# Performance work log

Hardware: AMD Instinct MI355X
Metric: run time of the kernel (lower is better)

Reference implementation:

```python
import jax, jax.numpy as jnp
import numpy as np

N = 100000
E = 6400000
H = 32  # num_hidden


def setup_inputs() -> dict:
    key = jax.random.key(0)
    ks = jax.random.split(key, 10)
    x = jax.random.normal(ks[0], (N,), dtype=jnp.float32)
    u = jax.random.normal(ks[1], (N,), dtype=jnp.float32)
    edge_index = jax.random.randint(ks[2], (2, E), 0, N, dtype=jnp.int64)
    # MLP(2 -> H -> H -> 1), 3 linear layers with relu between
    def lin(k, fan_in, fan_out):
        bound = 1.0 / np.sqrt(fan_in)
        kw, kb = jax.random.split(k)
        W = jax.random.uniform(kw, (fan_in, fan_out), jnp.float32, -bound, bound)
        b = jax.random.uniform(kb, (fan_out,), jnp.float32, -bound, bound)
        return W, b
    W1, b1 = lin(ks[3], 2, H)
    W2, b2 = lin(ks[4], H, H)
    W3, b3 = lin(ks[5], H, 1)
    return {"x": x, "edge_index": edge_index, "u": u,
            "W1": W1, "b1": b1, "W2": W2, "b2": b2, "W3": W3, "b3": b3}


def reference(x, edge_index, u, W1, b1, W2, b2, W3, b3):
    src, dst = edge_index[0], edge_index[1]
    # gather node scalars, form per-edge feature [E, 2]
    x_edge = jnp.stack([x[src], x[dst]], axis=-1)
    # per-edge MLP: 2 -> H -> H -> 1 with relu
    h = jax.nn.relu(x_edge @ W1 + b1)
    h = jax.nn.relu(h @ W2 + b2)
    w = (h @ W3 + b3)[:, 0]  # [E]
    # spmm: f[i] = sum_{e: src[e]=i} w[e] * u[dst[e]]
    f = jax.ops.segment_sum(w * u[dst], src, num_segments=x.shape[0])
    return f
```

## Files before the change

kernel.cpp:

```cpp
#include <hip/hip_runtime.h>

#define H 32
#define NSEG 1000
#define RBITS 9
#define RANGE 512
#define SPLIT 10
#define SEGPER (NSEG / SPLIT)
#define MAXROWS 260
#define EBMAX 6400

typedef __attribute__((ext_vector_type(2))) __fp16 half2v;
typedef __attribute__((ext_vector_type(8))) __fp16 half8;
typedef __attribute__((ext_vector_type(4))) float f32x4;
typedef unsigned int u32;
typedef unsigned short u16;

union HU { int i[4]; half8 h; };

static __device__ __forceinline__ int pkrtz(float a, float b) {
    return __builtin_bit_cast(int, __builtin_amdgcn_cvt_pkrtz(a, b));
}

static __device__ __forceinline__ float fdot2f(int w, int ab, float c) {
    return __builtin_amdgcn_fdot2(__builtin_bit_cast(half2v, w),
                                  __builtin_bit_cast(half2v, ab), c, false);
}

struct Invar {
    int   w1p[8];
    float b1v[8];
    half8 afrag[2];
    f32x4 c0, c1;
    float w3lo[4], w3hi[4];
    float b3v;
};

static __device__ __forceinline__ void load_invar(
    Invar& v, int g, int col,
    const float* __restrict__ W1, const float* __restrict__ b1,
    const float* __restrict__ W2, const float* __restrict__ b2,
    const float* __restrict__ W3, const float* __restrict__ b3)
{
    const int klo = 4 * g, khi = 16 + 4 * g;
#pragma unroll
    for (int i = 0; i < 4; ++i) {
        v.w1p[i]     = pkrtz(W1[klo + i], W1[H + klo + i]);
        v.w1p[4 + i] = pkrtz(W1[khi + i], W1[H + khi + i]);
        v.b1v[i]     = b1[klo + i];
        v.b1v[4 + i] = b1[khi + i];
    }
#pragma unroll
    for (int mt = 0; mt < 2; ++mt) {
        HU ua;
        const int c = mt * 16 + col;
        ua.i[0] = pkrtz(W2[(klo + 0) * H + c], W2[(klo + 1) * H + c]);
        ua.i[1] = pkrtz(W2[(klo + 2) * H + c], W2[(klo + 3) * H + c]);
        ua.i[2] = pkrtz(W2[(khi + 0) * H + c], W2[(khi + 1) * H + c]);
        ua.i[3] = pkrtz(W2[(khi + 2) * H + c], W2[(khi + 3) * H + c]);
        v.afrag[mt] = ua.h;
    }
#pragma unroll
    for (int r = 0; r < 4; ++r) {
        v.c0[r] = b2[klo + r]; v.c1[r] = b2[khi + r];
        v.w3lo[r] = W3[klo + r]; v.w3hi[r] = W3[khi + r];
    }
    v.b3v = b3[0];
}

static __device__ __forceinline__ float edge_w(const Invar& v, int g, int col, int abpk)
{
    float wred0 = 0.f, wred1 = 0.f, wred2 = 0.f, wred3 = 0.f;
#pragma unroll
    for (int T = 0; T < 4; ++T) {
        const int abT = __builtin_amdgcn_ds_bpermute(((T << 4) + col) << 2, abpk);
        const float h0 = fmaxf(fdot2f(v.w1p[0], abT, v.b1v[0]), 0.f);
        const float h1 = fmaxf(fdot2f(v.w1p[1], abT, v.b1v[1]), 0.f);
        const float h2 = fmaxf(fdot2f(v.w1p[2], abT, v.b1v[2]), 0.f);
        const float h3 = fmaxf(fdot2f(v.w1p[3], abT, v.b1v[3]), 0.f);
        const float h4 = fmaxf(fdot2f(v.w1p[4], abT, v.b1v[4]), 0.f);
        const float h5 = fmaxf(fdot2f(v.w1p[5], abT, v.b1v[5]), 0.f);
        const float h6 = fmaxf(fdot2f(v.w1p[6], abT, v.b1v[6]), 0.f);
        const float h7 = fmaxf(fdot2f(v.w1p[7], abT, v.b1v[7]), 0.f);

        HU ub;
        ub.i[0] = pkrtz(h0, h1);
        ub.i[1] = pkrtz(h2, h3);
        ub.i[2] = pkrtz(h4, h5);
        ub.i[3] = pkrtz(h6, h7);

        f32x4 acc0 = __builtin_amdgcn_mfma_f32_16x16x32_f16(v.afrag[0], ub.h, v.c0, 0, 0, 0);
        f32x4 acc1 = __builtin_amdgcn_mfma_f32_16x16x32_f16(v.afrag[1], ub.h, v.c1, 0, 0, 0);

        float p = 0.f;
#pragma unroll
        for (int r = 0; r < 4; ++r) {
            p += fmaxf(acc0[r], 0.f) * v.w3lo[r];
            p += fmaxf(acc1[r], 0.f) * v.w3hi[r];
        }
        p += __shfl_xor(p, 16, 64);
        p += __shfl_xor(p, 32, 64);
        const float wt = p + v.b3v;
        if      (T == 0) wred0 = wt;
        else if (T == 1) wred1 = wt;
        else if (T == 2) wred2 = wt;
        else             wred3 = wt;
    }
    const float wa = (g & 1) ? wred1 : wred0;
    const float wb = (g & 1) ? wred3 : wred2;
    return (g & 2) ? wb : wa;
}

__global__ void xu_pack_kernel(const float* __restrict__ x, const float* __restrict__ u,
                               float2* __restrict__ xu, int n) {
    int i = blockIdx.x * 256 + threadIdx.x;
    if (i < n) xu[i] = make_float2(x[i], u[i]);
}

__global__ __launch_bounds__(256) void p1_kernel(
    const float* __restrict__ x,
    const int*   __restrict__ ei,
    const float2* __restrict__ xu,
    const float* __restrict__ W1, const float* __restrict__ b1,
    const float* __restrict__ W2, const float* __restrict__ b2,
    const float* __restrict__ W3, const float* __restrict__ b3,
    u32* __restrict__ pairs, u32* __restrict__ offs,
    int E, int Eb, int nbuk)
{
    __shared__ u32 cnt[MAXROWS];
    __shared__ u32 cur[MAXROWS];
    __shared__ u32 wsum[4];
    __shared__ u32 lds_pairs[EBMAX];
    const int tid  = threadIdx.x;
    const int lane = tid & 63;
    const int wv   = tid >> 6;
    const int g    = lane >> 4;
    const int col  = lane & 15;
    const int b    = blockIdx.x;

    const int slice0 = b * Eb;
    int sliceN = E - slice0;
    if (sliceN < 0) sliceN = 0;
    if (sliceN > Eb) sliceN = Eb;

    Invar v;
    load_invar(v, g, col, W1, b1, W2, b2, W3, b3);

    for (int k = tid; k <= nbuk; k += 256) cnt[k] = 0;
    __syncthreads();
    if (((slice0 & 3) == 0) && ((sliceN & 3) == 0)) {
        const uint4* e4 = (const uint4*)(ei + slice0);
        const int n4 = sliceN >> 2;
        for (int i = tid; i < n4; i += 256) {
            const uint4 s4 = e4[i];
            atomicAdd(&cnt[s4.x >> RBITS], 1u);
            atomicAdd(&cnt[s4.y >> RBITS], 1u);
            atomicAdd(&cnt[s4.z >> RBITS], 1u);
            atomicAdd(&cnt[s4.w >> RBITS], 1u);
        }
    } else {
        for (int i = tid; i < sliceN; i += 256)
            atomicAdd(&cnt[((u32)ei[slice0 + i]) >> RBITS], 1u);
    }
    __syncthreads();

    {
        const u32 myc = (tid < nbuk) ? cnt[tid] : 0;
        u32 val = myc;
#pragma unroll
        for (int d = 1; d < 64; d <<= 1) {
            const u32 t = __shfl_up(val, d, 64);
            if (lane >= d) val += t;
        }
        if (lane == 63) wsum[wv] = val;
        __syncthreads();
        u32 woff = 0;
#pragma unroll
        for (int w = 0; w < 4; ++w) if (w < wv) woff += wsum[w];
        val += woff;
        if (tid < nbuk) cur[tid] = val - myc;
        if (tid == 0)   cur[nbuk] = wsum[0] + wsum[1] + wsum[2] + wsum[3];
    }
    __syncthreads();
    for (int k = tid; k <= nbuk; k += 256) offs[(size_t)k * NSEG + b] = cur[k];
    __syncthreads();

    const int nbfull = sliceN >> 6;
    const int nquad  = nbfull >> 2;
    for (int q = wv; q < nquad; q += 4) {
        const int e0 = slice0 + (q << 8) + lane;
        const int e1 = e0 + 64, e2 = e0 + 128, e3 = e0 + 192;
        const int src0 = ei[e0],     src1 = ei[e1],     src2 = ei[e2],     src3 = ei[e3];
        const int dst0 = ei[E + e0], dst1 = ei[E + e1], dst2 = ei[E + e2], dst3 = ei[E + e3];
        const float  x0  = x[src0],  x1  = x[src1],  x2  = x[src2],  x3  = x[src3];
        const float2 xd0 = xu[dst0], xd1 = xu[dst1], xd2 = xu[dst2], xd3 = xu[dst3];

        const float w0 = edge_w(v, g, col, pkrtz(x0, xd0.x));
        const float w1 = edge_w(v, g, col, pkrtz(x1, xd1.x));
        const float w2 = edge_w(v, g, col, pkrtz(x2, xd2.x));
        const float w3 = edge_w(v, g, col, pkrtz(x3, xd3.x));

        const u32 pos0 = atomicAdd(&cur[((u32)src0) >> RBITS], 1u);
        lds_pairs[pos0] = ((u32)(u16)pkrtz(w0 * xd0.y, 0.0f)) | (((u32)src0 & (RANGE - 1)) << 16);
        const u32 pos1 = atomicAdd(&cur[((u32)src1) >> RBITS], 1u);
        lds_pairs[pos1] = ((u32)(u16)pkrtz(w1 * xd1.y, 0.0f)) | (((u32)src1 & (RANGE - 1)) << 16);
        const u32 pos2 = atomicAdd(&cur[((u32)src2) >> RBITS], 1u);
        lds_pairs[pos2] = ((u32)(u16)pkrtz(w2 * xd2.y, 0.0f)) | (((u32)src2 & (RANGE - 1)) << 16);
        const u32 pos3 = atomicAdd(&cur[((u32)src3) >> RBITS], 1u);
        lds_pairs[pos3] = ((u32)(u16)pkrtz(w3 * xd3.y, 0.0f)) | (((u32)src3 & (RANGE - 1)) << 16);
    }
    const int nbany = (sliceN + 63) >> 6;
    for (int bi = (nquad << 2) + wv; bi < nbany; bi += 4) {
        const int loc = (bi << 6) + lane;
        const bool valid = loc < sliceN;
        const int eL = slice0 + (valid ? loc : 0);
        const int src = ei[eL];
        const int dst = ei[E + eL];
        const float2 xud = xu[dst];
        const int abpk = pkrtz(x[src], xud.x);
        const float we = edge_w(v, g, col, abpk);
        if (valid) {
            const int buk = ((u32)src) >> RBITS;
            const u32 pos = atomicAdd(&cur[buk], 1u);
            lds_pairs[pos] = ((u32)(u16)pkrtz(we * xud.y, 0.0f)) | (((u32)src & (RANGE - 1)) << 16);
        }
    }
    __syncthreads();

    const int n4 = sliceN >> 2;
    const uint4* lp4 = (const uint4*)lds_pairs;
    uint4* gp4 = (uint4*)(pairs + slice0);
    for (int i = tid; i < n4; i += 256) gp4[i] = lp4[i];
    for (int i = (n4 << 2) + tid; i < sliceN; i += 256) pairs[slice0 + i] = lds_pairs[i];
}

__global__ __launch_bounds__(256) void p2_kernel(
    const u32* __restrict__ pairs, const u32* __restrict__ offs,
    float* __restrict__ pf, int Eb, int nbuk)
{
    __shared__ float acc[RANGE];
    __shared__ u32 so_l[SEGPER];
    __shared__ u32 pre[SEGPER + 1];
    __shared__ u32 wsum[4];
    const int tid = threadIdx.x;
    const int lane = tid & 63;
    const int wv  = tid >> 6;
    const int buk = blockIdx.x / SPLIT;
    const int sp  = blockIdx.x % SPLIT;

    acc[tid] = 0.f;
    acc[tid + 256] = 0.f;
    u32 myc = 0, so = 0;
    if (tid < SEGPER) {
        const int s = sp + tid * SPLIT;
        so  = offs[(size_t)buk * NSEG + s];
        myc = offs[(size_t)(buk + 1) * NSEG + s] - so;
    }
    {
        u32 val = myc;
#pragma unroll
        for (int d = 1; d < 64; d <<= 1) {
            const u32 t = __shfl_up(val, d, 64);
            if (lane >= d) val += t;
        }
        if (lane == 63) wsum[wv] = val;
        __syncthreads();
        u32 woff = 0;
#pragma unroll
        for (int w = 0; w < 4; ++w) if (w < wv) woff += wsum[w];
        val += woff;
        if (tid < SEGPER) { so_l[tid] = so; pre[tid + 1] = val; }
        if (tid == 0) pre[0] = 0;
    }
    __syncthreads();

    const int total = (int)pre[SEGPER];
    for (int base = tid << 2; base < total; base += 1024) {
#pragma unroll
        for (int k = 0; k < 4; ++k) {
            const int i = base + k;
            if (i >= total) break;
            int lo = 0, hi = SEGPER;
            while (hi - lo > 1) {
                const int mid = (lo + hi) >> 1;
                if (pre[mid] <= (u32)i) lo = mid; else hi = mid;
            }
            const int s = sp + lo * SPLIT;
            const u32 p = pairs[(size_t)s * Eb + so_l[lo] + (u32)i - pre[lo]];
            const float val = (float)__builtin_bit_cast(_Float16, (u16)(p & 0xffffu));
            atomicAdd(&acc[p >> 16], val);
        }
    }
    __syncthreads();

    const size_t stride = (size_t)nbuk * RANGE;
    const int node0 = buk * RANGE;
    pf[(size_t)sp * stride + node0 + tid] = acc[tid];
    pf[(size_t)sp * stride + node0 + tid + 256] = acc[tid + 256];
}

__global__ void freduce_kernel(const float* __restrict__ pf, float* __restrict__ f,
                               int n, int stride) {
    const int i = blockIdx.x * 256 + threadIdx.x;
    if (i >= n) return;
    float s = 0.f;
#pragma unroll
    for (int r = 0; r < SPLIT; ++r) s += pf[(size_t)r * stride + i];
    f[i] = s;
}

__global__ void zero_kernel(float* __restrict__ p, int n) {
    int i = blockIdx.x * blockDim.x + threadIdx.x;
    if (i < n) p[i] = 0.0f;
}

__global__ __launch_bounds__(256) void fb_kernel(
    const float* __restrict__ x,
    const int*   __restrict__ ei,
    const float* __restrict__ u,
    const float* __restrict__ W1, const float* __restrict__ b1,
    const float* __restrict__ W2, const float* __restrict__ b2,
    const float* __restrict__ W3, const float* __restrict__ b3,
    float* __restrict__ f, int E)
{
    const int lane = threadIdx.x & 63;
    const int g    = lane >> 4;
    const int col  = lane & 15;

    Invar v;
    load_invar(v, g, col, W1, b1, W2, b2, W3, b3);

    const int nbatch = E >> 6;
    const int gw = blockIdx.x * 4 + (threadIdx.x >> 6);
    const int nw = gridDim.x * 4;
    for (int bt = gw; bt < nbatch; bt += nw) {
        const int e   = (bt << 6) + lane;
        const int src = ei[e];
        const int dst = ei[E + e];
        const int abpk = pkrtz(x[src], x[dst]);
        const float ud = u[dst];
        const float we = edge_w(v, g, col, abpk);
        atomicAdd(&f[src], we * ud);
    }
}

extern "C" void kernel_launch(void* const* d_in, const int* in_sizes, int n_in,
                              void* d_out, int out_size, void* d_ws, size_t ws_size,
                              hipStream_t stream) {
    const float* x  = (const float*)d_in[0];
    const int*   ei = (const int*)d_in[1];
    const float* u  = (const float*)d_in[2];
    const float* W1 = (const float*)d_in[3];
    const float* b1 = (const float*)d_in[4];
    const float* W2 = (const float*)d_in[5];
    const float* b2 = (const float*)d_in[6];
    const float* W3 = (const float*)d_in[7];
    const float* b3 = (const float*)d_in[8];
    float* f = (float*)d_out;

    const int n = in_sizes[0];
    const int E = in_sizes[1] / 2;

    const int nbuk = (n + RANGE - 1) / RANGE;
    const int Eb = (((E + NSEG - 1) / NSEG) + 63) & ~63;
    const size_t stride = (size_t)nbuk * RANGE;
    const size_t need = ((size_t)NSEG * Eb + (size_t)(nbuk + 1) * NSEG + (size_t)SPLIT * stride)
                        * sizeof(u32);
    const bool xu_fits = (size_t)SPLIT * stride * sizeof(float) >= (size_t)n * sizeof(float2);

    if (nbuk + 1 <= MAXROWS && nbuk <= 256 && Eb <= EBMAX && ws_size >= need
        && (E & 63) == 0 && xu_fits) {
        u32* pairs = (u32*)d_ws;
        u32* offs  = pairs + (size_t)NSEG * Eb;
        float* pf  = (float*)(offs + (size_t)(nbuk + 1) * NSEG);
        float2* xu = (float2*)pf;

        xu_pack_kernel<<<(n + 255) / 256, 256, 0, stream>>>(x, u, xu, n);
        p1_kernel<<<NSEG, 256, 0, stream>>>(x, ei, xu, W1, b1, W2, b2, W3, b3,
                                            pairs, offs, E, Eb, nbuk);
        p2_kernel<<<nbuk * SPLIT, 256, 0, stream>>>(pairs, offs, pf, Eb, nbuk);
        freduce_kernel<<<(n + 255) / 256, 256, 0, stream>>>(pf, f, n, (int)stride);
    } else {
        zero_kernel<<<(n + 255) / 256, 256, 0, stream>>>(f, n);
        fb_kernel<<<2048, 256, 0, stream>>>(x, ei, u, W1, b1, W2, b2, W3, b3, f, E);
    }
}
```

Before: 127.4 us.

## Split fused MLP+bucket-sort kernel into separate MLP and sort kernels

The fused p1 kernel, which computed per-edge MLP weights and bucket-sorted them in LDS, is split in two. A new mlp_kernel runs without the large LDS footprint on 2048 blocks and writes packed fp16 values to global memory. A separate sort_kernel then reads src and those values back and scatters them into bucket order. This aims to raise occupancy for the compute-heavy MLP (the 25KB LDS array limited blocks per CU), at the cost of an extra 4-byte-per-edge global write and read plus one more launch.

Result: slower. 140.0 us (+9.9%).

```diff
diff --git a/kernel.cpp b/kernel.cpp
--- a/kernel.cpp
+++ b/kernel.cpp
@@ -116,14 +116,60 @@
     if (i < n) xu[i] = make_float2(x[i], u[i]);
 }
 
-__global__ __launch_bounds__(256) void p1_kernel(
+__global__ __launch_bounds__(256) void mlp_kernel(
     const float* __restrict__ x,
     const int*   __restrict__ ei,
     const float2* __restrict__ xu,
     const float* __restrict__ W1, const float* __restrict__ b1,
     const float* __restrict__ W2, const float* __restrict__ b2,
     const float* __restrict__ W3, const float* __restrict__ b3,
-    u32* __restrict__ pairs, u32* __restrict__ offs,
+    u32* __restrict__ wval,
+    int E)
+{
+    const int lane = threadIdx.x & 63;
+    const int g    = lane >> 4;
+    const int col  = lane & 15;
+
+    Invar v;
+    load_invar(v, g, col, W1, b1, W2, b2, W3, b3);
+
+    const int nquad = E >> 8;
+    const int gw = blockIdx.x * 4 + (threadIdx.x >> 6);
+    const int nw = gridDim.x * 4;
+
+    for (int q = gw; q < nquad; q += nw) {
+        const int e0 = (q << 8) + lane;
+        const int e1 = e0 + 64, e2 = e0 + 128, e3 = e0 + 192;
+        const int src0 = ei[e0],     src1 = ei[e1],     src2 = ei[e2],     src3 = ei[e3];
+        const int dst0 = ei[E + e0], dst1 = ei[E + e1], dst2 = ei[E + e2], dst3 = ei[E + e3];
+        const float  x0  = x[src0],  x1  = x[src1],  x2  = x[src2],  x3  = x[src3];
+        const float2 xd0 = xu[dst0], xd1 = xu[dst1], xd2 = xu[dst2], xd3 = xu[dst3];
+
+        const float w0 = edge_w(v, g, col, pkrtz(x0, xd0.x));
+        const float w1 = edge_w(v, g, col, pkrtz(x1, xd1.x));
+        const float w2 = edge_w(v, g, col, pkrtz(x2, xd2.x));
+        const float w3 = edge_w(v, g, col, pkrtz(x3, xd3.x));
+
+        wval[e0] = (u32)(u16)pkrtz(w0 * xd0.y, 0.0f);
+        wval[e1] = (u32)(u16)pkrtz(w1 * xd1.y, 0.0f);
+        wval[e2] = (u32)(u16)pkrtz(w2 * xd2.y, 0.0f);
+        wval[e3] = (u32)(u16)pkrtz(w3 * xd3.y, 0.0f);
+    }
+    const int ngrp = E >> 6;
+    for (int bt = (nquad << 2) + gw; bt < ngrp; bt += nw) {
+        const int e   = (bt << 6) + lane;
+        const int src = ei[e];
+        const int dst = ei[E + e];
+        const float2 xd = xu[dst];
+        const float we = edge_w(v, g, col, pkrtz(x[src], xd.x));
+        wval[e] = (u32)(u16)pkrtz(we * xd.y, 0.0f);
+    }
+}
+
+__global__ __launch_bounds__(256) void sort_kernel(
+    const int* __restrict__ ei,
+    u32* __restrict__ pairs,
+    u32* __restrict__ offs,
     int E, int Eb, int nbuk)
 {
     __shared__ u32 cnt[MAXROWS];
@@ -133,17 +179,12 @@
     const int tid  = threadIdx.x;
     const int lane = tid & 63;
     const int wv   = tid >> 6;
-    const int g    = lane >> 4;
-    const int col  = lane & 15;
     const int b    = blockIdx.x;
 
     const int slice0 = b * Eb;
     int sliceN = E - slice0;
     if (sliceN < 0) sliceN = 0;
     if (sliceN > Eb) sliceN = Eb;
-
-    Invar v;
-    load_invar(v, g, col, W1, b1, W2, b2, W3, b3);
 
     for (int k = tid; k <= nbuk; k += 256) cnt[k] = 0;
     __syncthreads();
@@ -184,53 +225,38 @@
     for (int k = tid; k <= nbuk; k += 256) offs[(size_t)k * NSEG + b] = cur[k];
     __syncthreads();
 
-    const int nbfull = sliceN >> 6;
-    const int nquad  = nbfull >> 2;
-    for (int q = wv; q < nquad; q += 4) {
-        const int e0 = slice0 + (q << 8) + lane;
-        const int e1 = e0 + 64, e2 = e0 + 128, e3 = e0 + 192;
-        const int src0 = ei[e0],     src1 = ei[e1],     src2 = ei[e2],     src3 = ei[e3];
-        const int dst0 = ei[E + e0], dst1 = ei[E + e1], dst2 = ei[E + e2], dst3 = ei[E + e3];
-        const float  x0  = x[src0],  x1  = x[src1],  x2  = x[src2],  x3  = x[src3];
-        const float2 xd0 = xu[dst0], xd1 = xu[dst1], xd2 = xu[dst2], xd3 = xu[dst3];
-
-        const float w0 = edge_w(v, g, col, pkrtz(x0, xd0.x));
-        const float w1 = edge_w(v, g, col, pkrtz(x1, xd1.x));
-        const float w2 = edge_w(v, g, col, pkrtz(x2, xd2.x));
-        const float w3 = edge_w(v, g, col, pkrtz(x3, xd3.x));
-
-        const u32 pos0 = atomicAdd(&cur[((u32)src0) >> RBITS], 1u);
-        lds_pairs[pos0] = ((u32)(u16)pkrtz(w0 * xd0.y, 0.0f)) | (((u32)src0 & (RANGE - 1)) << 16);
-        const u32 pos1 = atomicAdd(&cur[((u32)src1) >> RBITS], 1u);
-        lds_pairs[pos1] = ((u32)(u16)pkrtz(w1 * xd1.y, 0.0f)) | (((u32)src1 & (RANGE - 1)) << 16);
-        const u32 pos2 = atomicAdd(&cur[((u32)src2) >> RBITS], 1u);
-        lds_pairs[pos2] = ((u32)(u16)pkrtz(w2 * xd2.y, 0.0f)) | (((u32)src2 & (RANGE - 1)) << 16);
-        const u32 pos3 = atomicAdd(&cur[((u32)src3) >> RBITS], 1u);
-        lds_pairs[pos3] = ((u32)(u16)pkrtz(w3 * xd3.y, 0.0f)) | (((u32)src3 & (RANGE - 1)) << 16);
-    }
-    const int nbany = (sliceN + 63) >> 6;
-    for (int bi = (nquad << 2) + wv; bi < nbany; bi += 4) {
-        const int loc = (bi << 6) + lane;
-        const bool valid = loc < sliceN;
-        const int eL = slice0 + (valid ? loc : 0);
-        const int src = ei[eL];
-        const int dst = ei[E + eL];
-        const float2 xud = xu[dst];
-        const int abpk = pkrtz(x[src], xud.x);
-        const float we = edge_w(v, g, col, abpk);
-        if (valid) {
-            const int buk = ((u32)src) >> RBITS;
-            const u32 pos = atomicAdd(&cur[buk], 1u);
-            lds_pairs[pos] = ((u32)(u16)pkrtz(we * xud.y, 0.0f)) | (((u32)src & (RANGE - 1)) << 16);
-        }
-    }
-    __syncthreads();
-
-    const int n4 = sliceN >> 2;
+    if (((slice0 & 3) == 0) && ((sliceN & 3) == 0)) {
+        const uint4* e4 = (const uint4*)(ei + slice0);
+        const uint4* w4 = (const uint4*)(pairs + slice0);
+        const int n4 = sliceN >> 2;
+        for (int i = tid; i < n4; i += 256) {
+            const uint4 s4 = e4[i];
+            const uint4 v4 = w4[i];
+            u32 pos;
+            pos = atomicAdd(&cur[s4.x >> RBITS], 1u);
+            lds_pairs[pos] = (v4.x & 0xffffu) | ((s4.x & (RANGE - 1)) << 16);
+            pos = atomicAdd(&cur[s4.y >> RBITS], 1u);
+            lds_pairs[pos] = (v4.y & 0xffffu) | ((s4.y & (RANGE - 1)) << 16);
+            pos = atomicAdd(&cur[s4.z >> RBITS], 1u);
+            lds_pairs[pos] = (v4.z & 0xffffu) | ((s4.z & (RANGE - 1)) << 16);
+            pos = atomicAdd(&cur[s4.w >> RBITS], 1u);
+            lds_pairs[pos] = (v4.w & 0xffffu) | ((s4.w & (RANGE - 1)) << 16);
+        }
+    } else {
+        for (int i = tid; i < sliceN; i += 256) {
+            const u32 src = (u32)ei[slice0 + i];
+            const u32 vv  = pairs[slice0 + i];
+            const u32 pos = atomicAdd(&cur[src >> RBITS], 1u);
+            lds_pairs[pos] = (vv & 0xffffu) | ((src & (RANGE - 1)) << 16);
+        }
+    }
+    __syncthreads();
+
+    const int n4d = sliceN >> 2;
     const uint4* lp4 = (const uint4*)lds_pairs;
     uint4* gp4 = (uint4*)(pairs + slice0);
-    for (int i = tid; i < n4; i += 256) gp4[i] = lp4[i];
-    for (int i = (n4 << 2) + tid; i < sliceN; i += 256) pairs[slice0 + i] = lds_pairs[i];
+    for (int i = tid; i < n4d; i += 256) gp4[i] = lp4[i];
+    for (int i = (n4d << 2) + tid; i < sliceN; i += 256) pairs[slice0 + i] = lds_pairs[i];
 }
 
 __global__ __launch_bounds__(256) void p2_kernel(
@@ -375,8 +401,9 @@
         float2* xu = (float2*)pf;
 
         xu_pack_kernel<<<(n + 255) / 256, 256, 0, stream>>>(x, u, xu, n);
-        p1_kernel<<<NSEG, 256, 0, stream>>>(x, ei, xu, W1, b1, W2, b2, W3, b3,
-                                            pairs, offs, E, Eb, nbuk);
+        mlp_kernel<<<2048, 256, 0, stream>>>(x, ei, xu, W1, b1, W2, b2, W3, b3,
+                                             pairs, E);
+        sort_kernel<<<NSEG, 256, 0, stream>>>(ei, pairs, offs, E, Eb, nbuk);
         p2_kernel<<<nbuk * SPLIT, 256, 0, stream>>>(pairs, offs, pf, Eb, nbuk);
         freduce_kernel<<<(n + 255) / 256, 256, 0, stream>>>(pf, f, n, (int)stride);
     } else {
```
